# Kernel tuning notes

Measured on AMD Instinct MI355X. Metric: run time of the kernel, lower is better.

## Reference

```python
import jax, jax.numpy as jnp
import numpy as np

VTH = 1.0      # v_threshold
TAU = 2.0      # spikingjelly LIFNode default tau
ALPHA = 2.0    # ATan surrogate alpha
EPS = 1e-5     # BatchNorm eps
N_HEADS = 8
TOPK = 4       # routed regions per query region
REGION = 64    # tokens per region (4096 tokens -> 64 regions)


@jax.custom_vjp
def spike_fn(v):
    return (v >= VTH).astype(v.dtype)

def _spike_fwd(v):
    return (v >= VTH).astype(v.dtype), v

def _spike_bwd(v, g):
    sg = (ALPHA / 2.0) / (1.0 + (jnp.pi / 2.0 * ALPHA * (v - VTH)) ** 2)
    return (g * sg,)

spike_fn.defvjp(_spike_fwd, _spike_bwd)


def lif(x):
    # x: [T, B, L, D]; LIF with decay_input=True, hard reset to 0, detach_reset
    def step(v, xt):
        v = v + (xt - v) / TAU
        s = spike_fn(v)
        v = v * (1.0 - jax.lax.stop_gradient(s))
        return v, s
    _, s = jax.lax.scan(step, jnp.zeros_like(x[0]), x)
    return s


def batchnorm(x, gamma, beta):
    # torch BN1d over [T*B, D, L] in training mode == per-channel stats over (T,B,L)
    mean = x.mean(axis=(0, 1, 2))
    var = jnp.mean((x - mean) ** 2, axis=(0, 1, 2))
    return (x - mean) * jax.lax.rsqrt(var + EPS) * gamma + beta


def bilevel_attn(x, qkv_w, qkv_b, proj_w, proj_b):
    # x: [TB, L, D]
    TB, L, D = x.shape
    nreg = L // REGION
    hd = D // N_HEADS
    qkv = x @ qkv_w.T + qkv_b
    q, k, v = jnp.split(qkv, 3, axis=-1)
    qr = q.reshape(TB, nreg, REGION, D)
    kr = k.reshape(TB, nreg, REGION, D)
    vr = v.reshape(TB, nreg, REGION, D)
    # coarse region-level routing via mean-pooled q/k affinity
    aff = jnp.einsum('bnd,bmd->bnm', qr.mean(2), kr.mean(2))  # [TB, nreg, nreg]
    _, idx = jax.lax.top_k(aff, TOPK)                         # [TB, nreg, TOPK]
    gather = jax.vmap(lambda t, ix: t[ix])                    # per-sample region gather
    kg = gather(kr, idx).reshape(TB, nreg, TOPK * REGION, N_HEADS, hd)
    vg = gather(vr, idx).reshape(TB, nreg, TOPK * REGION, N_HEADS, hd)
    qh = qr.reshape(TB, nreg, REGION, N_HEADS, hd)
    logits = jnp.einsum('bnqhd,bnkhd->bnhqk', qh, kg) * (hd ** -0.5)
    p = jax.nn.softmax(logits, axis=-1)
    o = jnp.einsum('bnhqk,bnkhd->bnqhd', p, vg).reshape(TB, L, D)
    return o @ proj_w.T + proj_b


def setup_inputs() -> dict:
    key = jax.random.key(0)
    ks = jax.random.split(key, 8)
    T, B, Lt, L, D = 4, 2, 4, 1024, 256
    Ltot = Lt * L
    s = 0.02
    return {
        'x': jax.random.normal(ks[0], (T, B, Ltot, D), jnp.float32),
        'bn1_g': jnp.ones((D,), jnp.float32),
        'bn1_b': jnp.zeros((D,), jnp.float32),
        'bn2_g': jnp.ones((D,), jnp.float32),
        'bn2_b': jnp.zeros((D,), jnp.float32),
        'qkv_w': jax.random.normal(ks[1], (3 * D, D), jnp.float32) * s,
        'qkv_b': jnp.zeros((3 * D,), jnp.float32),
        'proj_w': jax.random.normal(ks[2], (D, D), jnp.float32) * s,
        'proj_b': jnp.zeros((D,), jnp.float32),
        'ffn_w1': jax.random.normal(ks[3], (4 * D, D), jnp.float32) * s,
        'ffn_b1': jnp.zeros((4 * D,), jnp.float32),
        'ffn_w2': jax.random.normal(ks[4], (D, 4 * D), jnp.float32) * s,
        'ffn_b2': jnp.zeros((D,), jnp.float32),
        'scale': jnp.ones((1,), jnp.float32) * 0.5,
        'Lt': Lt, 'b': B, 'L': L, 'dim': D,
    }


def reference(x, bn1_g, bn1_b, bn2_g, bn2_b, qkv_w, qkv_b, proj_w, proj_b,
              ffn_w1, ffn_b1, ffn_w2, ffn_b2, scale, Lt, b, L, dim):
    T = x.shape[0]
    Ltot = Lt * L
    # attention branch
    identity = x
    s1 = lif(batchnorm(x, bn1_g, bn1_b))
    a = bilevel_attn(s1.reshape(T * b, Ltot, dim), qkv_w, qkv_b, proj_w, proj_b)
    x = identity + a.reshape(T, b, Ltot, dim) * scale
    # ffn branch
    s2 = lif(batchnorm(x, bn2_g, bn2_b))
    h = jax.nn.gelu(s2 @ ffn_w1.T + ffn_b1, approximate=False) @ ffn_w2.T + ffn_b2
    return x + h * scale
```

## Files before the change

kernel.cpp:

```cpp
#include <hip/hip_runtime.h>
#include <hip/hip_bf16.h>
#include <math.h>

typedef __attribute__((ext_vector_type(8))) short short8;
typedef __attribute__((ext_vector_type(4))) float f32x4;

#define DIM 256
#define NROWS 32768
#define PERT 2097152
#define SAMP_TOK 4096

__device__ __forceinline__ float b2f(__hip_bfloat16 h){ return __bfloat162float(h); }
__device__ __forceinline__ __hip_bfloat16 f2b(float f){ return __float2bfloat16(f); }
__device__ __forceinline__ unsigned short f2bu(float f){
  __hip_bfloat16 h = __float2bfloat16(f);
  unsigned short u; __builtin_memcpy(&u, &h, 2); return u;
}

__global__ void f2b_k(const float* __restrict__ in, __hip_bfloat16* __restrict__ out, int n){
  int i = blockIdx.x * 256 + threadIdx.x;
  if (i < n) out[i] = f2b(in[i]);
}

__global__ void bn_stats_k(const float* __restrict__ x, float* __restrict__ sum, float* __restrict__ sumsq){
  int c = threadIdx.x;
  size_t base = (size_t)blockIdx.x * 256 * DIM + c;
  float s = 0.f, s2 = 0.f;
  for (int i = 0; i < 256; ++i){
    float v = x[base + (size_t)i * DIM];
    s += v; s2 += v * v;
  }
  atomicAdd(&sum[c], s);
  atomicAdd(&sumsq[c], s2);
}

__global__ void bn_fin_k(const float* __restrict__ sum, const float* __restrict__ sumsq,
                         const float* __restrict__ g, const float* __restrict__ b,
                         float* __restrict__ a_out, float* __restrict__ b_out){
  int c = threadIdx.x;
  float mean = sum[c] * (1.f/32768.f);
  float var  = sumsq[c] * (1.f/32768.f) - mean*mean;
  float a = g[c] / sqrtf(var + 1e-5f);
  a_out[c] = a;
  b_out[c] = b[c] - mean * a;
}

__global__ void lif_k(const float* __restrict__ x, const float* __restrict__ av,
                      const float* __restrict__ bv, __hip_bfloat16* __restrict__ s){
  int e = blockIdx.x * blockDim.x + threadIdx.x;
  if (e >= PERT) return;
  int c = e & (DIM - 1);
  float a = av[c], b = bv[c];
  float v = 0.f;
  #pragma unroll
  for (int t = 0; t < 4; ++t){
    float xn = x[(size_t)t * PERT + e] * a + b;
    v += (xn - v) * 0.5f;
    float sp = (v >= 1.0f) ? 1.0f : 0.0f;
    s[(size_t)t * PERT + e] = f2b(sp);
    v = (v >= 1.0f) ? 0.f : v;
  }
}

__global__ void region_sum_k(const __hip_bfloat16* __restrict__ s, float* __restrict__ sm){
  int r = blockIdx.x, c = threadIdx.x;
  float acc = 0.f;
  size_t base = (size_t)r * 64 * DIM + c;
  for (int i = 0; i < 64; ++i) acc += b2f(s[base + (size_t)i * DIM]);
  sm[(size_t)r * DIM + c] = acc * 0.015625f;
}

__global__ void rgemm_k(const float* __restrict__ smr, const float* __restrict__ w,
                        const float* __restrict__ bias, float* __restrict__ qkm){
  __shared__ float arow[256];
  int r = blockIdx.x, t = threadIdx.x;
  arow[t] = smr[(size_t)r * 256 + t];
  __syncthreads();
  for (int j = t; j < 512; j += 256){
    const float* wr = w + (size_t)j * 256;
    float acc = 0.f;
    for (int k = 0; k < 256; ++k) acc += arow[k] * wr[k];
    qkm[(size_t)r * 512 + j] = acc + bias[j];
  }
}

template<int EPI>
__global__ __launch_bounds__(256) void gemm_bt(
    const __hip_bfloat16* __restrict__ A, const __hip_bfloat16* __restrict__ W,
    const float* __restrict__ bias, void* __restrict__ outp,
    const void* __restrict__ extra, const float* __restrict__ scaleptr,
    int K, int N)
{
  const int LDT = 40;
  __shared__ __align__(16) short As[128 * 40];
  __shared__ __align__(16) short Ws[128 * 40];
  int tid = threadIdx.x;
  int bm = blockIdx.x, bn = blockIdx.y;
  int srow = tid >> 2;
  int scol = (tid & 3) << 3;
  int lane = tid & 63;
  int l16 = lane & 15, quad = lane >> 4;
  int wv = tid >> 6;
  int wm = (wv >> 1) << 6, wn = (wv & 1) << 6;

  f32x4 zero = {0.f, 0.f, 0.f, 0.f};
  f32x4 acc[4][4];
  #pragma unroll
  for (int i = 0; i < 4; ++i)
    #pragma unroll
    for (int j = 0; j < 4; ++j) acc[i][j] = zero;

  for (int k0 = 0; k0 < K; k0 += 32){
    #pragma unroll
    for (int p = 0; p < 2; ++p){
      int r = (p << 6) + srow;
      *reinterpret_cast<uint4*>(&As[r * LDT + scol]) =
        *reinterpret_cast<const uint4*>(A + (size_t)(bm * 128 + r) * K + k0 + scol);
      *reinterpret_cast<uint4*>(&Ws[r * LDT + scol]) =
        *reinterpret_cast<const uint4*>(W + (size_t)(bn * 128 + r) * K + k0 + scol);
    }
    __syncthreads();
    short8 af[4];
    #pragma unroll
    for (int mi = 0; mi < 4; ++mi)
      af[mi] = *reinterpret_cast<const short8*>(&As[(wm + mi * 16 + l16) * LDT + (quad << 3)]);
    #pragma unroll
    for (int ni = 0; ni < 4; ++ni){
      short8 bfr = *reinterpret_cast<const short8*>(&Ws[(wn + ni * 16 + l16) * LDT + (quad << 3)]);
      #pragma unroll
      for (int mi = 0; mi < 4; ++mi)
        acc[mi][ni] = __builtin_amdgcn_mfma_f32_16x16x32_bf16(af[mi], bfr, acc[mi][ni], 0, 0, 0);
    }
    __syncthreads();
  }

  float sc = 0.f;
  if (EPI == 1 || EPI == 3) sc = scaleptr[0];
  #pragma unroll
  for (int ni = 0; ni < 4; ++ni){
    int colg = (bn << 7) + wn + ni * 16 + l16;
    float bvl = bias[colg];
    #pragma unroll
    for (int mi = 0; mi < 4; ++mi){
      #pragma unroll
      for (int r = 0; r < 4; ++r){
        int rowg = (bm << 7) + wm + mi * 16 + (quad << 2) + r;
        float v = acc[mi][ni][r] + bvl;
        size_t off = (size_t)rowg * N + colg;
        if (EPI == 0){
          ((__hip_bfloat16*)outp)[off] = f2b(v);
        } else if (EPI == 1){
          ((float*)outp)[off] = ((const float*)extra)[off] + v * sc;
        } else if (EPI == 2){
          float gl = 0.5f * v * (1.0f + erff(v * 0.70710678118654752f));
          ((__hip_bfloat16*)outp)[off] = f2b(gl);
        } else {
          ((float*)outp)[off] = ((const float*)extra)[off] + v * sc;
        }
      }
    }
  }
}

__global__ void topk_k(const float* __restrict__ qkm, int* __restrict__ idx){
  __shared__ float aff[64];
  int r = blockIdx.x;
  int m = threadIdx.x;
  int b = r >> 6;
  const float4* qrow = reinterpret_cast<const float4*>(qkm + (size_t)r * 512);
  const float4* krow = reinterpret_cast<const float4*>(qkm + (size_t)(b * 64 + m) * 512 + 256);
  float dot = 0.f;
  for (int d = 0; d < 64; ++d){
    float4 qv = qrow[d], kv = krow[d];
    dot += qv.x * kv.x + qv.y * kv.y + qv.z * kv.z + qv.w * kv.w;
  }
  aff[m] = dot;
  __syncthreads();
  if (m == 0){
    #pragma unroll
    for (int t = 0; t < 4; ++t){
      float best = -INFINITY; int bi = 0;
      for (int i = 0; i < 64; ++i){
        if (aff[i] > best){ best = aff[i]; bi = i; }
      }
      aff[bi] = -INFINITY;
      idx[r * 4 + t] = bi;
    }
  }
}

__global__ __launch_bounds__(256) void attn_mfma_k(
    const __hip_bfloat16* __restrict__ qkv, const int* __restrict__ idx,
    __hip_bfloat16* __restrict__ o_out, int rbase)
{
  __shared__ __align__(16) short lds[27136];
  __shared__ float den_s[4][16];
  const int rl = blockIdx.x;
  const int h  = blockIdx.y;
  const int rg = rbase + rl;
  const int bl = rl >> 6;
  const int tid = threadIdx.x;
  const int w = tid >> 6, lane = tid & 63;
  const int l16 = lane & 15, quad = lane >> 4;
  short* Pw = lds + 10240 + w * 4224;

  const int reg = idx[rg * 4 + (tid >> 6)] & 63;
  const size_t srow = (size_t)bl * SAMP_TOK + (size_t)reg * 64 + (tid & 63);
  const __hip_bfloat16* kvsrc = qkv + srow * 768 + 256 + (size_t)h * 32;

  const size_t qrow = (size_t)rl * 64 + w * 16 + l16;
  short8 qf = *reinterpret_cast<const short8*>(qkv + qrow * 768 + (size_t)h * 32 + quad * 8);

  uint4 vreg[4];
  #pragma unroll
  for (int c = 0; c < 4; ++c)
    vreg[c] = *reinterpret_cast<const uint4*>(kvsrc + 256 + c * 8);

  #pragma unroll
  for (int c = 0; c < 4; ++c)
    *reinterpret_cast<uint4*>(&lds[tid * 40 + c * 8]) =
      *reinterpret_cast<const uint4*>(kvsrc + c * 8);
  __syncthreads();

  f32x4 s[16];
  #pragma unroll
  for (int nt = 0; nt < 16; ++nt){
    short8 bf = *reinterpret_cast<const short8*>(&lds[(nt * 16 + l16) * 40 + quad * 8]);
    f32x4 z = {0.f, 0.f, 0.f, 0.f};
    s[nt] = __builtin_amdgcn_mfma_f32_16x16x32_bf16(qf, bf, z, 0, 0, 0);
  }
  __syncthreads();

  #pragma unroll
  for (int c = 0; c < 4; ++c){
    short8 vv = *reinterpret_cast<short8*>(&vreg[c]);
    #pragma unroll
    for (int e = 0; e < 8; ++e)
      lds[(c * 8 + e) * 264 + tid] = vv[e];
  }

  float m4[4] = {-1e30f, -1e30f, -1e30f, -1e30f};
  #pragma unroll
  for (int nt = 0; nt < 16; ++nt)
    #pragma unroll
    for (int r = 0; r < 4; ++r) m4[r] = fmaxf(m4[r], s[nt][r]);
  #pragma unroll
  for (int xm = 1; xm < 16; xm <<= 1)
    #pragma unroll
    for (int r = 0; r < 4; ++r) m4[r] = fmaxf(m4[r], __shfl_xor(m4[r], xm));
  float d4[4] = {0.f, 0.f, 0.f, 0.f};
  #pragma unroll
  for (int nt = 0; nt < 16; ++nt)
    #pragma unroll
    for (int r = 0; r < 4; ++r){
      float e = __expf((s[nt][r] - m4[r]) * 0.17677669529663687f);
      s[nt][r] = e; d4[r] += e;
    }
  #pragma unroll
  for (int xm = 1; xm < 16; xm <<= 1)
    #pragma unroll
    for (int r = 0; r < 4; ++r) d4[r] += __shfl_xor(d4[r], xm);
  if (l16 == 0){
    #pragma unroll
    for (int r = 0; r < 4; ++r) den_s[w][quad * 4 + r] = d4[r];
  }
  #pragma unroll
  for (int nt = 0; nt < 16; ++nt)
    #pragma unroll
    for (int r = 0; r < 4; ++r)
      Pw[(quad * 4 + r) * 264 + nt * 16 + l16] = (short)f2bu(s[nt][r]);
  __syncthreads();

  f32x4 o0 = {0.f, 0.f, 0.f, 0.f}, o1 = o0;
  #pragma unroll
  for (int kk = 0; kk < 8; ++kk){
    short8 pb = *reinterpret_cast<const short8*>(&Pw[l16 * 264 + kk * 32 + quad * 8]);
    short8 a0 = *reinterpret_cast<const short8*>(&lds[l16 * 264 + kk * 32 + quad * 8]);
    short8 a1 = *reinterpret_cast<const short8*>(&lds[(16 + l16) * 264 + kk * 32 + quad * 8]);
    o0 = __builtin_amdgcn_mfma_f32_16x16x32_bf16(a0, pb, o0, 0, 0, 0);
    o1 = __builtin_amdgcn_mfma_f32_16x16x32_bf16(a1, pb, o1, 0, 0, 0);
  }
  float inv = 1.f / den_s[w][l16];
  size_t obase = ((size_t)rl * 64 + w * 16 + l16) * 256 + (size_t)h * 32;
  unsigned pk0 = (unsigned)f2bu(o0[0] * inv) | ((unsigned)f2bu(o0[1] * inv) << 16);
  unsigned pk1 = (unsigned)f2bu(o0[2] * inv) | ((unsigned)f2bu(o0[3] * inv) << 16);
  unsigned pk2 = (unsigned)f2bu(o1[0] * inv) | ((unsigned)f2bu(o1[1] * inv) << 16);
  unsigned pk3 = (unsigned)f2bu(o1[2] * inv) | ((unsigned)f2bu(o1[3] * inv) << 16);
  *reinterpret_cast<uint2*>(o_out + obase + quad * 4)      = make_uint2(pk0, pk1);
  *reinterpret_cast<uint2*>(o_out + obase + 16 + quad * 4) = make_uint2(pk2, pk3);
}

extern "C" void kernel_launch(void* const* d_in, const int* in_sizes, int n_in,
                              void* d_out, int out_size, void* d_ws, size_t ws_size,
                              hipStream_t stream)
{
  const float* x      = (const float*)d_in[0];
  const float* bn1_g  = (const float*)d_in[1];
  const float* bn1_b  = (const float*)d_in[2];
  const float* bn2_g  = (const float*)d_in[3];
  const float* bn2_b  = (const float*)d_in[4];
  const float* qkv_w  = (const float*)d_in[5];
  const float* qkv_b  = (const float*)d_in[6];
  const float* proj_w = (const float*)d_in[7];
  const float* proj_b = (const float*)d_in[8];
  const float* ffn_w1 = (const float*)d_in[9];
  const float* ffn_b1 = (const float*)d_in[10];
  const float* ffn_w2 = (const float*)d_in[11];
  const float* ffn_b2 = (const float*)d_in[12];
  const float* scale  = (const float*)d_in[13];
  float* x2 = (float*)d_out;

  char* ws = (char*)d_ws;
  const size_t MB = 1024 * 1024;
  float* sum1 = (float*)(ws + 0);
  float* sq1  = (float*)(ws + 1024);
  float* sum2 = (float*)(ws + 2048);
  float* sq2  = (float*)(ws + 3072);
  float* a1   = (float*)(ws + 4096);
  float* b1   = (float*)(ws + 5120);
  float* a2   = (float*)(ws + 6144);
  float* b2   = (float*)(ws + 7168);
  int*   idxb = (int*)(ws + 8192);
  float* smr  = (float*)(ws + 16384);
  float* qkm  = (float*)(ws + 540672);
  __hip_bfloat16* qkv_wb  = (__hip_bfloat16*)(ws + 1589248);
  __hip_bfloat16* proj_wb = (__hip_bfloat16*)(ws + 1982464);
  __hip_bfloat16* ffn_w1b = (__hip_bfloat16*)(ws + 2113536);
  __hip_bfloat16* ffn_w2b = (__hip_bfloat16*)(ws + 2637824);
  __hip_bfloat16* s1 = (__hip_bfloat16*)(ws + 4 * MB);
  __hip_bfloat16* s2 = s1;
  char* chunkbuf = ws + 20 * MB;

  size_t avail = (ws_size > 20 * MB) ? (ws_size - 20 * MB) : (8 * MB);
  int nc = (avail >= 64 * MB) ? 8 : (avail >= 32 * MB) ? 4 : (avail >= 16 * MB) ? 2 : 1;
  int crows = 32768;
  while ((size_t)crows * 2048 > avail && crows > 2048) crows >>= 1;

  __hip_bfloat16* qkvc = (__hip_bfloat16*)chunkbuf;
  __hip_bfloat16* oc   = (__hip_bfloat16*)(chunkbuf + (size_t)nc * 6 * MB);
  __hip_bfloat16* h1   = (__hip_bfloat16*)chunkbuf;

  hipMemsetAsync(d_ws, 0, 4096, stream);

  f2b_k<<<(196608 + 255) / 256, 256, 0, stream>>>(qkv_w, qkv_wb, 196608);
  f2b_k<<<(65536 + 255) / 256, 256, 0, stream>>>(proj_w, proj_wb, 65536);
  f2b_k<<<(262144 + 255) / 256, 256, 0, stream>>>(ffn_w1, ffn_w1b, 262144);
  f2b_k<<<(262144 + 255) / 256, 256, 0, stream>>>(ffn_w2, ffn_w2b, 262144);

  bn_stats_k<<<128, 256, 0, stream>>>(x, sum1, sq1);
  bn_fin_k<<<1, 256, 0, stream>>>(sum1, sq1, bn1_g, bn1_b, a1, b1);
  lif_k<<<PERT / 256, 256, 0, stream>>>(x, a1, b1, s1);
  region_sum_k<<<512, 256, 0, stream>>>(s1, smr);
  rgemm_k<<<512, 256, 0, stream>>>(smr, qkv_w, qkv_b, qkm);
  topk_k<<<512, 64, 0, stream>>>(qkm, idxb);

  const int nchunkA = 8 / nc;
  for (int c = 0; c < nchunkA; ++c){
    const size_t ro = (size_t)c * nc * SAMP_TOK;
    gemm_bt<0><<<dim3(nc * SAMP_TOK / 128, 6), 256, 0, stream>>>(
        s1 + ro * 256, qkv_wb, qkv_b, qkvc, nullptr, nullptr, 256, 768);
    attn_mfma_k<<<dim3(nc * 64, 8), 256, 0, stream>>>(qkvc, idxb, oc, c * nc * 64);
    gemm_bt<1><<<dim3(nc * SAMP_TOK / 128, 2), 256, 0, stream>>>(
        oc, proj_wb, proj_b, x2 + ro * 256, x + ro * 256, scale, 256, 256);
  }

  bn_stats_k<<<128, 256, 0, stream>>>(x2, sum2, sq2);
  bn_fin_k<<<1, 256, 0, stream>>>(sum2, sq2, bn2_g, bn2_b, a2, b2);
  lif_k<<<PERT / 256, 256, 0, stream>>>(x2, a2, b2, s2);
  const int nchunkF = 32768 / crows;
  for (int c = 0; c < nchunkF; ++c){
    const size_t ro = (size_t)c * crows;
    gemm_bt<2><<<dim3(crows / 128, 8), 256, 0, stream>>>(
        s2 + ro * 256, ffn_w1b, ffn_b1, h1, nullptr, nullptr, 256, 1024);
    gemm_bt<3><<<dim3(crows / 128, 2), 256, 0, stream>>>(
        h1, ffn_w2b, ffn_b2, x2 + ro * 256, x2 + ro * 256, scale, 1024, 256);
  }
}
```

Measured before the change: 383.1 us.

## Use direct global-to-LDS loads with swizzled layout and LDS-staged bf16 epilogue

The GEMM now loads A/W tiles with global_load_lds (16-byte direct-to-LDS) instead of going through registers. The LDS tiles are unpadded and XOR-style swizzled to avoid bank conflicts. The bf16-output epilogues (EPI 0/2) stage results through shared memory in two halves so each row is written to global memory as coalesced 16-byte stores instead of scattered 2-byte stores. This cuts register traffic and global write transactions, at the cost of extra barriers in the epilogue and reliance on the hardware's per-wave LDS placement rules for global_load_lds.

```diff
diff --git a/kernel.cpp b/kernel.cpp
--- a/kernel.cpp
+++ b/kernel.cpp
@@ -15,6 +15,12 @@
 __device__ __forceinline__ unsigned short f2bu(float f){
   __hip_bfloat16 h = __float2bfloat16(f);
   unsigned short u; __builtin_memcpy(&u, &h, 2); return u;
+}
+
+__device__ __forceinline__ void gl2lds16(const void* g, void* l){
+  __builtin_amdgcn_global_load_lds(
+      (const __attribute__((address_space(1))) unsigned int*)g,
+      (__attribute__((address_space(3))) unsigned int*)l, 16, 0, 0);
 }
 
 __global__ void f2b_k(const float* __restrict__ in, __hip_bfloat16* __restrict__ out, int n){
@@ -91,17 +97,37 @@
     const void* __restrict__ extra, const float* __restrict__ scaleptr,
     int K, int N)
 {
-  const int LDT = 40;
-  __shared__ __align__(16) short As[128 * 40];
-  __shared__ __align__(16) short Ws[128 * 40];
-  int tid = threadIdx.x;
-  int bm = blockIdx.x, bn = blockIdx.y;
-  int srow = tid >> 2;
-  int scol = (tid & 3) << 3;
-  int lane = tid & 63;
-  int l16 = lane & 15, quad = lane >> 4;
-  int wv = tid >> 6;
-  int wm = (wv >> 1) << 6, wn = (wv & 1) << 6;
+  __shared__ __align__(16) short smem[8192];
+  short* As = smem;
+  short* Ws = smem + 4096;
+  const int tid = threadIdx.x;
+  const int bm = blockIdx.x, bn = blockIdx.y;
+  const int lane = tid & 63;
+  const int l16 = lane & 15, quad = lane >> 4;
+  const int wv = tid >> 6;
+  const int wm = (wv >> 1) << 6, wn = (wv & 1) << 6;
+
+  const int sA0 = tid, sA1 = tid + 256;
+  const int r0 = sA0 >> 2, c0 = ((sA0 & 3) - r0) & 3;
+  const int r1 = sA1 >> 2, c1 = ((sA1 & 3) - r1) & 3;
+  const __hip_bfloat16* gA0 = A + (size_t)(bm * 128 + r0) * K + c0 * 8;
+  const __hip_bfloat16* gA1 = A + (size_t)(bm * 128 + r1) * K + c1 * 8;
+  const __hip_bfloat16* gB0 = W + (size_t)(bn * 128 + r0) * K + c0 * 8;
+  const __hip_bfloat16* gB1 = W + (size_t)(bn * 128 + r1) * K + c1 * 8;
+  const int wslot = tid & ~63;
+  short* ldsA0 = &As[(size_t)wslot * 8];
+  short* ldsA1 = &As[(size_t)(wslot + 256) * 8];
+  short* ldsB0 = &Ws[(size_t)wslot * 8];
+  short* ldsB1 = &Ws[(size_t)(wslot + 256) * 8];
+
+  int aoff[4], boff[4];
+  #pragma unroll
+  for (int i = 0; i < 4; ++i){
+    int ar = wm + i * 16 + l16;
+    aoff[i] = (ar * 4 + ((quad + ar) & 3)) * 8;
+    int br = wn + i * 16 + l16;
+    boff[i] = (br * 4 + ((quad + br) & 3)) * 8;
+  }
 
   f32x4 zero = {0.f, 0.f, 0.f, 0.f};
   f32x4 acc[4][4];
@@ -111,22 +137,18 @@
     for (int j = 0; j < 4; ++j) acc[i][j] = zero;
 
   for (int k0 = 0; k0 < K; k0 += 32){
-    #pragma unroll
-    for (int p = 0; p < 2; ++p){
-      int r = (p << 6) + srow;
-      *reinterpret_cast<uint4*>(&As[r * LDT + scol]) =
-        *reinterpret_cast<const uint4*>(A + (size_t)(bm * 128 + r) * K + k0 + scol);
-      *reinterpret_cast<uint4*>(&Ws[r * LDT + scol]) =
-        *reinterpret_cast<const uint4*>(W + (size_t)(bn * 128 + r) * K + k0 + scol);
-    }
+    gl2lds16(gA0 + k0, ldsA0);
+    gl2lds16(gA1 + k0, ldsA1);
+    gl2lds16(gB0 + k0, ldsB0);
+    gl2lds16(gB1 + k0, ldsB1);
     __syncthreads();
     short8 af[4];
     #pragma unroll
     for (int mi = 0; mi < 4; ++mi)
-      af[mi] = *reinterpret_cast<const short8*>(&As[(wm + mi * 16 + l16) * LDT + (quad << 3)]);
+      af[mi] = *reinterpret_cast<const short8*>(&As[aoff[mi]]);
     #pragma unroll
     for (int ni = 0; ni < 4; ++ni){
-      short8 bfr = *reinterpret_cast<const short8*>(&Ws[(wn + ni * 16 + l16) * LDT + (quad << 3)]);
+      short8 bfr = *reinterpret_cast<const short8*>(&Ws[boff[ni]]);
       #pragma unroll
       for (int mi = 0; mi < 4; ++mi)
         acc[mi][ni] = __builtin_amdgcn_mfma_f32_16x16x32_bf16(af[mi], bfr, acc[mi][ni], 0, 0, 0);
@@ -134,27 +156,48 @@
     __syncthreads();
   }
 
-  float sc = 0.f;
-  if (EPI == 1 || EPI == 3) sc = scaleptr[0];
-  #pragma unroll
-  for (int ni = 0; ni < 4; ++ni){
-    int colg = (bn << 7) + wn + ni * 16 + l16;
-    float bvl = bias[colg];
-    #pragma unroll
-    for (int mi = 0; mi < 4; ++mi){
+  if (EPI == 0 || EPI == 2){
+    #pragma unroll
+    for (int hh = 0; hh < 2; ++hh){
+      if ((wv >> 1) == hh){
+        #pragma unroll
+        for (int ni = 0; ni < 4; ++ni){
+          float bvl = bias[(bn << 7) + wn + ni * 16 + l16];
+          #pragma unroll
+          for (int mi = 0; mi < 4; ++mi){
+            #pragma unroll
+            for (int r = 0; r < 4; ++r){
+              float v = acc[mi][ni][r] + bvl;
+              if (EPI == 2) v = 0.5f * v * (1.0f + erff(v * 0.70710678118654752f));
+              smem[(mi * 16 + (quad << 2) + r) * 128 + wn + ni * 16 + l16] = (short)f2bu(v);
+            }
+          }
+        }
+      }
+      __syncthreads();
       #pragma unroll
-      for (int r = 0; r < 4; ++r){
-        int rowg = (bm << 7) + wm + mi * 16 + (quad << 2) + r;
-        float v = acc[mi][ni][r] + bvl;
-        size_t off = (size_t)rowg * N + colg;
-        if (EPI == 0){
-          ((__hip_bfloat16*)outp)[off] = f2b(v);
-        } else if (EPI == 1){
-          ((float*)outp)[off] = ((const float*)extra)[off] + v * sc;
-        } else if (EPI == 2){
-          float gl = 0.5f * v * (1.0f + erff(v * 0.70710678118654752f));
-          ((__hip_bfloat16*)outp)[off] = f2b(gl);
-        } else {
+      for (int i = 0; i < 4; ++i){
+        int s = tid + i * 256;
+        int row = s >> 4, cb = s & 15;
+        short8 val = *reinterpret_cast<const short8*>(&smem[row * 128 + cb * 8]);
+        *reinterpret_cast<short8*>((__hip_bfloat16*)outp +
+            (size_t)((bm << 7) + (hh << 6) + row) * N + (bn << 7) + cb * 8) = val;
+      }
+      __syncthreads();
+    }
+  } else {
+    const float sc = scaleptr[0];
+    #pragma unroll
+    for (int ni = 0; ni < 4; ++ni){
+      int colg = (bn << 7) + wn + ni * 16 + l16;
+      float bvl = bias[colg];
+      #pragma unroll
+      for (int mi = 0; mi < 4; ++mi){
+        #pragma unroll
+        for (int r = 0; r < 4; ++r){
+          int rowg = (bm << 7) + wm + mi * 16 + (quad << 2) + r;
+          float v = acc[mi][ni][r] + bvl;
+          size_t off = (size_t)rowg * N + colg;
           ((float*)outp)[off] = ((const float*)extra)[off] + v * sc;
         }
       }
```

Result: slower. 398.0 us (+3.9%).
